# Performance work log

Hardware: AMD Instinct MI355X
Metric: run time of the kernel (lower is better)

The kernel has to match this reference:

```python
import jax, jax.numpy as jnp
import numpy as np
from jax import lax

# --- static config (matches init_kwargs) ---
K_NAT, P_NAT, NHEAD, DM, L = 5, 2, 8, 128, 3
PK, OV, STRIDE = 4, 2, 2          # patcher kernel / overlap / stride = PK-OV
PPAD = PK - OV                    # circular pad for patcher/depatcher crop
RK, RC = 5, 12                    # res layer kernel, hidden channels = 3*4
DN = ('NCHW', 'OIHW', 'NCHW')


def setup_inputs() -> dict:
    key = jax.random.key(0)
    ks = jax.random.split(key, 16)
    B, C, H, W = 2, 3, 256, 256
    rn = lambda k, shape, s=0.02: jax.random.normal(k, shape, jnp.float32) * s
    return {
        'x': jax.random.normal(ks[0], (B, C, H, W), jnp.float32),
        'pos_w': jax.random.uniform(ks[1], (C, H, W), jnp.float32) + 0.5,
        'pos_b': jax.random.uniform(ks[2], (C, H, W), jnp.float32) - 0.5,
        'patch_w': rn(ks[3], (DM, C, PK, PK), 0.05),
        'patch_b': jnp.zeros((DM,), jnp.float32),
        'ln1_g': jnp.ones((L, DM), jnp.float32),
        'ln1_b': jnp.zeros((L, DM), jnp.float32),
        'qkv_w': rn(ks[4], (L, 3 * DM, DM)),
        'qkv_b': jnp.zeros((L, 3 * DM), jnp.float32),
        'rpb': rn(ks[5], (L, NHEAD, 2 * K_NAT - 1, 2 * K_NAT - 1)),
        'proj_w': rn(ks[6], (L, DM, DM)),
        'proj_b': jnp.zeros((L, DM), jnp.float32),
        'ln2_g': jnp.ones((L, DM), jnp.float32),
        'ln2_b': jnp.zeros((L, DM), jnp.float32),
        'fc1_w': rn(ks[7], (L, 4 * DM, DM)),
        'fc1_b': jnp.zeros((L, 4 * DM), jnp.float32),
        'fc2_w': rn(ks[8], (L, DM, 4 * DM)),
        'fc2_b': jnp.zeros((L, DM), jnp.float32),
        'depatch_w': rn(ks[9], (DM, C, PK, PK), 0.05),   # ConvTranspose2d weight (Cin,Cout,kh,kw)
        'depatch_b': jnp.zeros((C,), jnp.float32),
        'res_cv1_w': rn(ks[10], (RC, C, RK, RK), 0.05),
        'res_cv1_b': jnp.zeros((RC,), jnp.float32),
        'res_cv2_w': rn(ks[11], (C, RC, 1, 1), 0.05),
        'res_cv2_b': jnp.zeros((C,), jnp.float32),
    }


def _layer_norm(x, g, b):
    m = x.mean(-1, keepdims=True)
    v = x.var(-1, keepdims=True)
    return (x - m) * lax.rsqrt(v + 1e-5) * g + b


def _nat_block(x, ln1_g, ln1_b, qkv_w, qkv_b, rpb, proj_w, proj_b,
               ln2_g, ln2_b, fc1_w, fc1_b, fc2_w, fc2_b):
    # x: (B,H,W,C). NATLayer: LN -> circular pad by k//2 -> NA -> crop -> residual -> LN -> MLP -> residual.
    # After padding, every kept (interior) pixel has a full centered kxk neighborhood,
    # so we compute q only at interior positions and gather kxk K/V windows from the padded map.
    B, H, W, C = x.shape
    k, p, h = K_NAT, P_NAT, NHEAD
    dh = C // h
    y = _layer_norm(x, ln1_g, ln1_b)
    y = jnp.pad(y, ((0, 0), (p, p), (p, p), (0, 0)), mode='wrap')  # circular
    qkv = y @ qkv_w.T + qkv_b                                      # (B,H+2p,W+2p,3C)
    q, kk, vv = jnp.split(qkv, 3, axis=-1)
    q = q[:, p:p + H, p:p + W].reshape(B, H, W, h, dh) * (dh ** -0.5)
    def win(t):
        t = t.reshape(B, H + 2 * p, W + 2 * p, h, dh)
        return jnp.stack([t[:, i:i + H, j:j + W]
                          for i in range(k) for j in range(k)], axis=3)  # (B,H,W,k*k,h,dh)
    kw, vw = win(kk), win(vv)
    bias = rpb[:, p:p + k, p:p + k].reshape(h, k * k)  # centered slice of (2k-1,2k-1) RPB
    logits = jnp.einsum('bxyhd,bxynhd->bxyhn', q, kw) + bias
    a = jax.nn.softmax(logits, axis=-1)
    o = jnp.einsum('bxyhn,bxynhd->bxyhd', a, vw).reshape(B, H, W, C)
    x = x + (o @ proj_w.T + proj_b)
    y = _layer_norm(x, ln2_g, ln2_b)
    y = jax.nn.leaky_relu(y @ fc1_w.T + fc1_b) @ fc2_w.T + fc2_b
    return x + y


def _forward(x, pos_w, pos_b, patch_w, patch_b, ln1_g, ln1_b, qkv_w, qkv_b,
             rpb, proj_w, proj_b, ln2_g, ln2_b, fc1_w, fc1_b, fc2_w, fc2_b,
             depatch_w, depatch_b, res_cv1_w, res_cv1_b, res_cv2_w, res_cv2_b):
    # positional embedding (dropout is identity, p=0)
    x = x * pos_w + pos_b
    # OverlapConvPatcher: circular pad by (PK-OV), conv kernel PK stride PK-OV -> (B,129,129,DM)
    xp = jnp.pad(x, ((0, 0), (0, 0), (PPAD, PPAD), (PPAD, PPAD)), mode='wrap')
    f = lax.conv_general_dilated(xp, patch_w, (STRIDE, STRIDE), 'VALID',
                                 dimension_numbers=DN) + patch_b[None, :, None, None]
    f = f.transpose(0, 2, 3, 1)
    for i in range(L):
        f = _nat_block(f, ln1_g[i], ln1_b[i], qkv_w[i], qkv_b[i], rpb[i],
                       proj_w[i], proj_b[i], ln2_g[i], ln2_b[i],
                       fc1_w[i], fc1_b[i], fc2_w[i], fc2_b[i])
    # OverlapDeconvDepatcher: ConvTranspose2d (kernel PK, stride PK-OV), crop PPAD border
    f = f.transpose(0, 3, 1, 2)
    wf = jnp.flip(depatch_w, (2, 3)).transpose(1, 0, 2, 3)  # (Cout,Cin,kh,kw)
    y = lax.conv_general_dilated(f, wf, (1, 1), [(PK - 1, PK - 1)] * 2,
                                 lhs_dilation=(STRIDE, STRIDE),
                                 dimension_numbers=DN) + depatch_b[None, :, None, None]
    y = y[:, :, PPAD:-PPAD, PPAD:-PPAD]  # (B,3,256,256)
    # ResLayer: circular-pad same conv 5x5 -> leaky_relu -> 1x1 conv -> residual
    yp = jnp.pad(y, ((0, 0), (0, 0), (RK // 2, RK // 2), (RK // 2, RK // 2)), mode='wrap')
    r = lax.conv_general_dilated(yp, res_cv1_w, (1, 1), 'VALID',
                                 dimension_numbers=DN) + res_cv1_b[None, :, None, None]
    r = jax.nn.leaky_relu(r)
    r = lax.conv_general_dilated(r, res_cv2_w, (1, 1), 'VALID',
                                 dimension_numbers=DN) + res_cv2_b[None, :, None, None]
    return y + r


def reference(x, pos_w, pos_b, patch_w, patch_b, ln1_g, ln1_b, qkv_w, qkv_b,
              rpb, proj_w, proj_b, ln2_g, ln2_b, fc1_w, fc1_b, fc2_w, fc2_b,
              depatch_w, depatch_b, res_cv1_w, res_cv1_b, res_cv2_w, res_cv2_b):
    return _forward(x, pos_w, pos_b, patch_w, patch_b, ln1_g, ln1_b, qkv_w, qkv_b,
                    rpb, proj_w, proj_b, ln2_g, ln2_b, fc1_w, fc1_b, fc2_w, fc2_b,
                    depatch_w, depatch_b, res_cv1_w, res_cv1_b, res_cv2_w, res_cv2_b)
```

## Files before the change

kernel.cpp:

```cpp
#include <hip/hip_runtime.h>
#include <hip/hip_bf16.h>
#include <math.h>

#define HF 129
#define WF 129
#define BDIM 2
#define TOK (BDIM*HF*WF)
#define DMOD 128
#define VTP 104

typedef __attribute__((ext_vector_type(8))) short short8;
typedef __attribute__((ext_vector_type(8))) unsigned short ushort8;
typedef __attribute__((ext_vector_type(4))) float f32x4;

__device__ __forceinline__ float leaky(float v){ return v > 0.f ? v : 0.01f*v; }
__device__ __forceinline__ float bf2f(unsigned short u){ return __uint_as_float(((unsigned int)u) << 16); }
__device__ __forceinline__ unsigned int f2bf(float f){
    unsigned int u = __float_as_uint(f);
    return (u + 0x7fff + ((u >> 16) & 1)) >> 16;
}

#define NQ 147456
#define NPJ 49152
#define N1 196608
#define N2 196608
#define NPAT 8192
#define NDEP 8192
__global__ __launch_bounds__(256) void prep_weights(
    const float* __restrict__ qkv_w, const float* __restrict__ proj_w,
    const float* __restrict__ fc1_w, const float* __restrict__ fc2_w,
    const float* __restrict__ patch_w, const float* __restrict__ dep_w,
    __hip_bfloat16* __restrict__ wq, __hip_bfloat16* __restrict__ wp,
    __hip_bfloat16* __restrict__ w1, __hip_bfloat16* __restrict__ w2,
    __hip_bfloat16* __restrict__ wpat, __hip_bfloat16* __restrict__ wdep,
    float* __restrict__ zero64)
{
    int off = blockIdx.x*256 + threadIdx.x;
    if (off < NQ) { wq[off] = __float2bfloat16(qkv_w[off]); return; } off -= NQ;
    if (off < NPJ){ wp[off] = __float2bfloat16(proj_w[off]); return; } off -= NPJ;
    if (off < N1) { w1[off] = __float2bfloat16(fc1_w[off]); return; } off -= N1;
    if (off < N2) { w2[off] = __float2bfloat16(fc2_w[off]); return; } off -= N2;
    if (off < NPAT){ int r = off>>6, e = off&63;
        wpat[off] = __float2bfloat16(e < 48 ? patch_w[r*48 + e] : 0.f); return; } off -= NPAT;
    if (off < NDEP){ int e = off>>7, d = off&127;
        wdep[off] = __float2bfloat16(e < 48 ? dep_w[d*48 + e] : 0.f); return; } off -= NDEP;
    if (off < 64) zero64[off] = 0.f;
}

__global__ __launch_bounds__(256) void im2col_kernel(
    const float* __restrict__ x, const float* __restrict__ pos_w, const float* __restrict__ pos_b,
    __hip_bfloat16* __restrict__ G)
{
    __shared__ float xs[12][260];
    int blk = blockIdx.x;
    int b = blk / HF, oh = blk - b*HF;
    int tid = threadIdx.x;
    #pragma unroll
    for (int it = 0; it < 3; ++it) {
        int p = it*4 + (tid >> 6);
        int c = p >> 2, r = p & 3;
        int h = (oh*2 + r - 2 + 256) & 255;
        int w4 = (tid & 63) * 4;
        float4 xv  = *(const float4*)(x     + ((size_t)(b*3 + c)*256 + h)*256 + w4);
        float4 pwv = *(const float4*)(pos_w + ((size_t)c*256 + h)*256 + w4);
        float4 pbv = *(const float4*)(pos_b + ((size_t)c*256 + h)*256 + w4);
        float4 o; o.x = xv.x*pwv.x + pbv.x; o.y = xv.y*pwv.y + pbv.y;
        o.z = xv.z*pwv.z + pbv.z; o.w = xv.w*pwv.w + pbv.w;
        *(float4*)&xs[p][w4] = o;
    }
    __syncthreads();
    int e = tid & 63, og = tid >> 6;
    int c = e >> 4, k = e & 15, kh = k >> 2, kw = k & 3;
    int p = c*4 + kh;
    unsigned short* Grow = (unsigned short*)G + (size_t)blk*WF*64;
    for (int ow = og; ow < WF; ow += 4) {
        unsigned short v = 0;
        if (e < 48) {
            int col = (ow*2 + kw - 2 + 256) & 255;
            v = (unsigned short)f2bf(xs[p][col]);
        }
        Grow[ow*64 + e] = v;
    }
}

template<int ACT, int RES, int OUTF, int LNE>
__global__ __launch_bounds__(256) void gemmF_kernel(
    const __hip_bfloat16* __restrict__ A, const __hip_bfloat16* __restrict__ W,
    const float* __restrict__ bias, const float* __restrict__ lng, const float* __restrict__ lnb,
    __hip_bfloat16* __restrict__ Cbf, float* __restrict__ Cf,
    __hip_bfloat16* __restrict__ yl, int M, int N, int K)
{
    __shared__ __align__(16) char As[64*128];
    __shared__ __align__(16) char Ws[128*128];
    __shared__ float2 lnred[64][2];
    int tid = threadIdx.x;
    int bm = blockIdx.x*64, bn = blockIdx.y*128;
    int lane = tid & 63, wid = tid >> 6;
    int wr = (wid >> 1)*32, wc = (wid & 1)*64;
    int lrow = lane & 15, lq = lane >> 4;
    int srow = tid >> 3, scg = tid & 7;
    int swz = (lrow & 7) << 4;
    int awo0 = ((srow     )*128 + scg*16) ^ ((srow&7)<<4);
    int awo1 = ((srow + 32)*128 + scg*16) ^ ((srow&7)<<4);

    bool v0 = (bm + srow) < M, v1 = (bm + srow + 32) < M;
    const __hip_bfloat16* a0p = A + (size_t)(bm + srow)*K + scg*8;
    const __hip_bfloat16* a1p = A + (size_t)(bm + srow + 32)*K + scg*8;
    const __hip_bfloat16* wp0 = W + (size_t)(bn + srow)*K + scg*8;

    f32x4 acc[2][4] = {};
    for (int k0 = 0; k0 < K; k0 += 64) {
        int4 va0 = {}, va1 = {};
        if (v0) va0 = *(const int4*)(a0p + k0);
        if (v1) va1 = *(const int4*)(a1p + k0);
        int4 vw0 = *(const int4*)(wp0 + k0);
        int4 vw1 = *(const int4*)(wp0 + (size_t)32*K + k0);
        int4 vw2 = *(const int4*)(wp0 + (size_t)64*K + k0);
        int4 vw3 = *(const int4*)(wp0 + (size_t)96*K + k0);
        __syncthreads();
        *(int4*)(As + awo0) = va0;
        *(int4*)(As + awo1) = va1;
        *(int4*)(Ws + awo0) = vw0;
        *(int4*)(Ws + awo1) = vw1;
        *(int4*)(Ws + (((srow+64)*128 + scg*16) ^ ((srow&7)<<4))) = vw2;
        *(int4*)(Ws + (((srow+96)*128 + scg*16) ^ ((srow&7)<<4))) = vw3;
        __syncthreads();
        #pragma unroll
        for (int ks = 0; ks < 2; ++ks) {
            int kb = ks*64;
            short8 af[2], bf[4];
            #pragma unroll
            for (int mi = 0; mi < 2; ++mi)
                af[mi] = *(const short8*)(As + (((wr + mi*16 + lrow)*128 + kb + lq*16) ^ swz));
            #pragma unroll
            for (int ni = 0; ni < 4; ++ni)
                bf[ni] = *(const short8*)(Ws + (((wc + ni*16 + lrow)*128 + kb + lq*16) ^ swz));
            #pragma unroll
            for (int mi = 0; mi < 2; ++mi)
                #pragma unroll
                for (int ni = 0; ni < 4; ++ni)
                    acc[mi][ni] = __builtin_amdgcn_mfma_f32_16x16x32_bf16(af[mi], bf[ni], acc[mi][ni], 0, 0, 0);
        }
    }
    float bcol[4];
    #pragma unroll
    for (int ni = 0; ni < 4; ++ni) bcol[ni] = bias[bn + wc + ni*16 + lrow];
    #pragma unroll
    for (int mi = 0; mi < 2; ++mi) {
        #pragma unroll
        for (int r = 0; r < 4; ++r) {
            int row = bm + wr + mi*16 + lq*4 + r;
            bool vrow = row < M;
            #pragma unroll
            for (int ni = 0; ni < 4; ++ni) {
                float v = acc[mi][ni][r] + bcol[ni];
                if (ACT) v = leaky(v);
                if (RES || OUTF) {
                    int col = wc + ni*16 + lrow;
                    size_t idx = (size_t)row*128 + col;
                    if (RES) { float old = vrow ? Cf[idx] : 0.f; v += old; }
                    if (vrow) Cf[idx] = v;
                } else {
                    int col = bn + wc + ni*16 + lrow;
                    if (vrow) Cbf[(size_t)row*N + col] = __float2bfloat16(v);
                }
                acc[mi][ni][r] = v;
            }
        }
    }
    if (LNE) {
        float sa[8], ssa[8];
        #pragma unroll
        for (int mi = 0; mi < 2; ++mi)
            #pragma unroll
            for (int r = 0; r < 4; ++r) {
                float s = 0.f, ss = 0.f;
                #pragma unroll
                for (int ni = 0; ni < 4; ++ni) { float v = acc[mi][ni][r]; s += v; ss += v*v; }
                sa[mi*4+r] = s; ssa[mi*4+r] = ss;
            }
        #pragma unroll
        for (int m = 1; m < 16; m <<= 1) {
            #pragma unroll
            for (int i = 0; i < 8; ++i) { sa[i] += __shfl_xor(sa[i], m); ssa[i] += __shfl_xor(ssa[i], m); }
        }
        if (lrow == 0) {
            #pragma unroll
            for (int i = 0; i < 8; ++i)
                lnred[wr + (i>>2)*16 + lq*4 + (i&3)][wc>>6] = make_float2(sa[i], ssa[i]);
        }
        __syncthreads();
        float gcol[4], bbcol[4];
        #pragma unroll
        for (int ni = 0; ni < 4; ++ni) {
            gcol[ni] = lng[wc + ni*16 + lrow];
            bbcol[ni] = lnb[wc + ni*16 + lrow];
        }
        #pragma unroll
        for (int mi = 0; mi < 2; ++mi) {
            #pragma unroll
            for (int r = 0; r < 4; ++r) {
                int rl = wr + mi*16 + lq*4 + r;
                int row = bm + rl;
                if (row >= M) continue;
                float2 h0 = lnred[rl][0], h1 = lnred[rl][1];
                float mean = (h0.x + h1.x) * (1.f/128.f);
                float var = (h0.y + h1.y) * (1.f/128.f) - mean*mean;
                float inv = rsqrtf(var + 1e-5f);
                #pragma unroll
                for (int ni = 0; ni < 4; ++ni) {
                    int col = wc + ni*16 + lrow;
                    float yv = (acc[mi][ni][r] - mean)*inv*gcol[ni] + bbcol[ni];
                    yl[(size_t)row*128 + col] = __float2bfloat16(yv);
                }
            }
        }
    }
}

__global__ __launch_bounds__(256) void attn_mfma_kernel(
    const __hip_bfloat16* __restrict__ qkv, const float* __restrict__ rpb,
    __hip_bfloat16* __restrict__ o)
{
    __shared__ __align__(16) char Kl[96*256];
    __shared__ __align__(16) char Vt[128*VTP*2];
    __shared__ __align__(16) char Pl[4][32*VTP*2];
    __shared__ float rpbl[8*81];
    int blk = blockIdx.x;
    int b = blk / (17*33);
    int rem = blk - b*(17*33);
    int tyi = rem / 33, txi = rem - tyi*33;
    int y0 = tyi*8, x0 = txi*4;
    int tid = threadIdx.x;
    int lane = tid & 63, wid = tid >> 6;
    int lrow = lane & 15, lq = lane >> 4;

    for (int u = tid; u < 648; u += 256) rpbl[u] = rpb[u];

    #pragma unroll
    for (int it = 0; it < 6; ++it) {
        int u = tid + it*256;
        int wtok = u >> 4, c = u & 15;
        int wy = wtok >> 3, wx = wtok & 7;
        int gy = y0 + wy - 2; gy += (gy < 0) ? HF : 0; gy -= (gy >= HF) ? HF : 0;
        int gx = x0 + wx - 2; gx += (gx < 0) ? WF : 0; gx -= (gx >= WF) ? WF : 0;
        size_t tk = (size_t)(b*HF + gy)*WF + gx;
        int4 v = *(const int4*)(qkv + tk*384 + 128 + c*8);
        *(int4*)(Kl + wtok*256 + ((c*16) ^ ((wtok & 7) << 4))) = v;
    }
    #pragma unroll
    for (int it = 0; it < 6; ++it) {
        int u = tid + it*256;
        int c = u / 96, wtok = u - c*96;
        int wy = wtok >> 3, wx = wtok & 7;
        int gy = y0 + wy - 2; gy += (gy < 0) ? HF : 0; gy -= (gy >= HF) ? HF : 0;
        int gx = x0 + wx - 2; gx += (gx < 0) ? WF : 0; gx -= (gx >= WF) ? WF : 0;
        size_t tk = (size_t)(b*HF + gy)*WF + gx;
        ushort8 v = *(const ushort8*)(qkv + tk*384 + 256 + c*8);
        unsigned short* dst = (unsigned short*)Vt + (c*8)*VTP + wtok;
        #pragma unroll
        for (int j = 0; j < 8; ++j) dst[j*VTP] = v[j];
    }
    __syncthreads();

    char* myP = Pl[wid];
    #pragma unroll
    for (int hh = 0; hh < 2; ++hh) {
        int h = wid + hh*4;
        short8 aq[2];
        #pragma unroll
        for (int mi = 0; mi < 2; ++mi) {
            int q = mi*16 + lrow;
            int ty = q >> 2, tx = q & 3;
            int gy = y0 + ty, gx = x0 + tx;
            int cy = gy < HF ? gy : HF-1, cx = gx < WF ? gx : WF-1;
            size_t tk = (size_t)(b*HF + cy)*WF + cx;
            short8 v = {};
            if (lq < 2) v = *(const short8*)(qkv + tk*384 + h*16 + lq*8);
            aq[mi] = v;
        }
        f32x4 sc[2][6];
        #pragma unroll
        for (int ni = 0; ni < 6; ++ni) {
            int krow = ni*16 + lrow;
            short8 bk = *(const short8*)(Kl + krow*256 + ((h*32 + (lq&1)*16) ^ ((krow&7)<<4)));
            f32x4 zz = {0.f,0.f,0.f,0.f};
            sc[0][ni] = __builtin_amdgcn_mfma_f32_16x16x32_bf16(aq[0], bk, zz, 0, 0, 0);
            sc[1][ni] = __builtin_amdgcn_mfma_f32_16x16x32_bf16(aq[1], bk, zz, 0, 0, 0);
        }
        int wxv = lrow & 7;
        int wyb = lrow >> 3;
        #pragma unroll
        for (int mi = 0; mi < 2; ++mi) {
            int tyq = mi*4 + lq;
            #pragma unroll
            for (int ni = 0; ni < 6; ++ni) {
                int dy = ni*2 + wyb - tyq;
                bool vdy = (dy >= 0) && (dy <= 4);
                int base = (dy + 2)*9 + wxv + 2;
                int cb = base < 3 ? 3 : (base > 80 ? 80 : base);
                const float* bp = rpbl + h*81 + cb - 3;
                float b0 = bp[0], b1 = bp[1], b2 = bp[2], b3 = bp[3];
                float bias_r[4] = {b3, b2, b1, b0};
                #pragma unroll
                for (int r = 0; r < 4; ++r) {
                    int dx = wxv - r;
                    bool ok = vdy && (dx >= 0) && (dx <= 4);
                    float s = sc[mi][ni][r]*0.25f + bias_r[r];
                    sc[mi][ni][r] = ok ? s : -1e30f;
                }
            }
        }
        float sum[8] = {};
        #pragma unroll
        for (int mi = 0; mi < 2; ++mi)
            #pragma unroll
            for (int ni = 0; ni < 6; ++ni)
                #pragma unroll
                for (int r = 0; r < 4; ++r) {
                    float p = __expf(sc[mi][ni][r]);
                    sc[mi][ni][r] = p;
                    sum[mi*4 + r] += p;
                }
        #pragma unroll
        for (int msk = 1; msk < 16; msk <<= 1)
            #pragma unroll
            for (int i = 0; i < 8; ++i) sum[i] += __shfl_xor(sum[i], msk);
        float inv[8];
        #pragma unroll
        for (int i = 0; i < 8; ++i) inv[i] = 1.f / sum[i];
        #pragma unroll
        for (int mi = 0; mi < 2; ++mi)
            #pragma unroll
            for (int ni = 0; ni < 6; ++ni)
                #pragma unroll
                for (int r = 0; r < 4; ++r) {
                    int q = mi*16 + lq*4 + r;
                    int w = ni*16 + lrow;
                    ((unsigned short*)myP)[q*VTP + w] =
                        (unsigned short)f2bf(sc[mi][ni][r]);
                }
        f32x4 ov[2] = {};
        #pragma unroll
        for (int kk = 0; kk < 3; ++kk) {
            short8 vb = *(const short8*)(Vt + (h*16 + lrow)*(VTP*2) + kk*64 + lq*16);
            #pragma unroll
            for (int mi = 0; mi < 2; ++mi) {
                short8 pa = *(const short8*)(myP + (mi*16 + lrow)*(VTP*2) + kk*64 + lq*16);
                ov[mi] = __builtin_amdgcn_mfma_f32_16x16x32_bf16(pa, vb, ov[mi], 0, 0, 0);
            }
        }
        #pragma unroll
        for (int mi = 0; mi < 2; ++mi) {
            int tyq = mi*4 + lq;
            int gy = y0 + tyq;
            #pragma unroll
            for (int r = 0; r < 4; ++r) {
                int gx = x0 + r;
                if (gy < HF && gx < WF) {
                    size_t tk = (size_t)(b*HF + gy)*WF + gx;
                    ((unsigned short*)o)[tk*128 + h*16 + lrow] =
                        (unsigned short)f2bf(ov[mi][r] * inv[mi*4 + r]);
                }
            }
        }
    }
}

template<int ACT, int RES, int OUTF, int A32>
__global__ __launch_bounds__(256) void mgemm_kernel(
    const void* __restrict__ Av, const __hip_bfloat16* __restrict__ W,
    const float* __restrict__ bias, __hip_bfloat16* __restrict__ Cbf,
    float* __restrict__ Cres, int M, int N, int K)
{
    __shared__ __align__(16) char As[64*128];
    __shared__ __align__(16) char Ws[64*128];
    int tid = threadIdx.x;
    int bm = blockIdx.x*64, bn = blockIdx.y*64;
    int lane = tid & 63, wid = tid >> 6;
    int wm = (wid >> 1)*32, wn = (wid & 1)*32;
    int lrow = lane & 15, lq = lane >> 4;
    int srow = tid >> 3, scg = tid & 7;
    int wo0 = ((srow     )*128 + scg*16) ^ ((srow&7)<<4);
    int wo1 = ((srow + 32)*128 + scg*16) ^ ((srow&7)<<4);
    int swz = (lrow & 7) << 4;
    int baseA0 = (wm + lrow     )*128 + lq*16;
    int baseA1 = (wm + 16 + lrow)*128 + lq*16;
    int baseB0 = (wn + lrow     )*128 + lq*16;
    int baseB1 = (wn + 16 + lrow)*128 + lq*16;

    f32x4 acc[2][2] = {};
    bool v0 = (bm + srow) < M, v1 = (bm + srow + 32) < M;
    const __hip_bfloat16* a0p = (const __hip_bfloat16*)Av + (size_t)(bm + srow)*K + scg*8;
    const __hip_bfloat16* a1p = (const __hip_bfloat16*)Av + (size_t)(bm + srow + 32)*K + scg*8;
    const float* a0pf = (const float*)Av + (size_t)(bm + srow)*K + scg*8;
    const float* a1pf = (const float*)Av + (size_t)(bm + srow + 32)*K + scg*8;
    const __hip_bfloat16* w0p = W + (size_t)(bn + srow)*K + scg*8;
    const __hip_bfloat16* w1p = W + (size_t)(bn + srow + 32)*K + scg*8;

    for (int k0 = 0; k0 < K; k0 += 64) {
        int4 va0 = {}, va1 = {};
        if (A32) {
            if (v0) {
                float4 p0 = *(const float4*)(a0pf + k0);
                float4 p1 = *(const float4*)(a0pf + k0 + 4);
                va0.x = (int)(f2bf(p0.x) | (f2bf(p0.y) << 16)); va0.y = (int)(f2bf(p0.z) | (f2bf(p0.w) << 16));
                va0.z = (int)(f2bf(p1.x) | (f2bf(p1.y) << 16)); va0.w = (int)(f2bf(p1.z) | (f2bf(p1.w) << 16));
            }
            if (v1) {
                float4 p0 = *(const float4*)(a1pf + k0);
                float4 p1 = *(const float4*)(a1pf + k0 + 4);
                va1.x = (int)(f2bf(p0.x) | (f2bf(p0.y) << 16)); va1.y = (int)(f2bf(p0.z) | (f2bf(p0.w) << 16));
                va1.z = (int)(f2bf(p1.x) | (f2bf(p1.y) << 16)); va1.w = (int)(f2bf(p1.z) | (f2bf(p1.w) << 16));
            }
        } else {
            if (v0) va0 = *(const int4*)(a0p + k0);
            if (v1) va1 = *(const int4*)(a1p + k0);
        }
        int4 vw0 = *(const int4*)(w0p + k0);
        int4 vw1 = *(const int4*)(w1p + k0);
        __syncthreads();
        *(int4*)(As + wo0) = va0;
        *(int4*)(As + wo1) = va1;
        *(int4*)(Ws + wo0) = vw0;
        *(int4*)(Ws + wo1) = vw1;
        __syncthreads();
        #pragma unroll
        for (int ks = 0; ks < 2; ++ks) {
            int kb = ks*64;
            short8 a0 = *(const short8*)(As + ((baseA0 + kb) ^ swz));
            short8 a1 = *(const short8*)(As + ((baseA1 + kb) ^ swz));
            short8 b0 = *(const short8*)(Ws + ((baseB0 + kb) ^ swz));
            short8 b1 = *(const short8*)(Ws + ((baseB1 + kb) ^ swz));
            acc[0][0] = __builtin_amdgcn_mfma_f32_16x16x32_bf16(a0, b0, acc[0][0], 0, 0, 0);
            acc[0][1] = __builtin_amdgcn_mfma_f32_16x16x32_bf16(a0, b1, acc[0][1], 0, 0, 0);
            acc[1][0] = __builtin_amdgcn_mfma_f32_16x16x32_bf16(a1, b0, acc[1][0], 0, 0, 0);
            acc[1][1] = __builtin_amdgcn_mfma_f32_16x16x32_bf16(a1, b1, acc[1][1], 0, 0, 0);
        }
    }
    float bv0 = bias[bn + wn + lrow];
    float bv1 = bias[bn + wn + 16 + lrow];
    #pragma unroll
    for (int mi = 0; mi < 2; ++mi) {
        #pragma unroll
        for (int r = 0; r < 4; ++r) {
            int row = bm + wm + mi*16 + lq*4 + r;
            if (row >= M) continue;
            #pragma unroll
            for (int ni = 0; ni < 2; ++ni) {
                float v = acc[mi][ni][r] + (ni ? bv1 : bv0);
                if (ACT == 1) v = leaky(v);
                int col = bn + wn + ni*16 + lrow;
                if (RES)       Cres[(size_t)row*N + col] += v;
                else if (OUTF) Cres[(size_t)row*N + col] = v;
                else           Cbf[(size_t)row*N + col] = __float2bfloat16(v);
            }
        }
    }
}

__global__ __launch_bounds__(256) void degather_kernel(const float* __restrict__ G,
    const float* __restrict__ db, float* __restrict__ yimg)
{
    int idx = blockIdx.x*256 + threadIdx.x;
    int b = idx >> 16;
    int pix = idx & 65535;
    int i = pix >> 8, j = pix & 255;
    int fh0 = i >> 1, fw0 = j >> 1;
    size_t r00 = ((size_t)(b*HF + fh0)*WF + fw0)*64;
    size_t r01 = r00 + 64;
    size_t r10 = r00 + (size_t)WF*64;
    size_t r11 = r10 + 64;
    int wr0 = (2 + (i & 1))*4, wr1 = (i & 1)*4;
    int wc0 = 2 + (j & 1), wc1 = (j & 1);
    #pragma unroll
    for (int c = 0; c < 3; ++c) {
        int e = c*16;
        float v = db[c]
                + G[r00 + e + wr0 + wc0] + G[r01 + e + wr0 + wc1]
                + G[r10 + e + wr1 + wc0] + G[r11 + e + wr1 + wc1];
        yimg[((size_t)(b*3 + c) << 16) + pix] = v;
    }
}

__global__ __launch_bounds__(256) void res_kernel(const float* __restrict__ y,
    const float* __restrict__ w1, const float* __restrict__ b1,
    const float* __restrict__ w2, const float* __restrict__ b2, float* __restrict__ out)
{
    int idx = blockIdx.x*256 + threadIdx.x;
    int b = idx >> 16;
    int pix = idx & 65535;
    int i = pix >> 8, j = pix & 255;
    float yv[3][5][5];
    #pragma unroll
    for (int c = 0; c < 3; ++c) {
        #pragma unroll
        for (int u = 0; u < 5; ++u) {
            int ii = (i + u - 2 + 256) & 255;
            #pragma unroll
            for (int v = 0; v < 5; ++v) {
                int jj = (j + v - 2 + 256) & 255;
                yv[c][u][v] = y[((size_t)(b*3 + c)*256 + ii)*256 + jj];
            }
        }
    }
    float r1[12];
    #pragma unroll
    for (int rc = 0; rc < 12; ++rc) {
        float a = b1[rc];
        #pragma unroll
        for (int c = 0; c < 3; ++c)
            #pragma unroll
            for (int u = 0; u < 5; ++u)
                #pragma unroll
                for (int v = 0; v < 5; ++v)
                    a += yv[c][u][v] * w1[rc*75 + c*25 + u*5 + v];
        r1[rc] = leaky(a);
    }
    #pragma unroll
    for (int c = 0; c < 3; ++c) {
        float a = b2[c];
        #pragma unroll
        for (int rc = 0; rc < 12; ++rc) a += r1[rc]*w2[c*12 + rc];
        out[((size_t)(b*3 + c)*256 + i)*256 + j] = yv[c][2][2] + a;
    }
}

extern "C" void kernel_launch(void* const* d_in, const int* in_sizes, int n_in,
                              void* d_out, int out_size, void* d_ws, size_t ws_size,
                              hipStream_t stream)
{
    const float* x      = (const float*)d_in[0];
    const float* pos_w  = (const float*)d_in[1];
    const float* pos_b  = (const float*)d_in[2];
    const float* patch_w= (const float*)d_in[3];
    const float* patch_b= (const float*)d_in[4];
    const float* ln1_g  = (const float*)d_in[5];
    const float* ln1_b  = (const float*)d_in[6];
    const float* qkv_w  = (const float*)d_in[7];
    const float* qkv_b  = (const float*)d_in[8];
    const float* rpb    = (const float*)d_in[9];
    const float* proj_w = (const float*)d_in[10];
    const float* proj_b = (const float*)d_in[11];
    const float* ln2_g  = (const float*)d_in[12];
    const float* ln2_b  = (const float*)d_in[13];
    const float* fc1_w  = (const float*)d_in[14];
    const float* fc1_b  = (const float*)d_in[15];
    const float* fc2_w  = (const float*)d_in[16];
    const float* fc2_b  = (const float*)d_in[17];
    const float* dep_w  = (const float*)d_in[18];
    const float* dep_b  = (const float*)d_in[19];
    const float* rc1_w  = (const float*)d_in[20];
    const float* rc1_b  = (const float*)d_in[21];
    const float* rc2_w  = (const float*)d_in[22];
    const float* rc2_b  = (const float*)d_in[23];

    const size_t SZ = (size_t)TOK * 128;
    char* w = (char*)d_ws;
    float* f            = (float*)w;            w += SZ*4;
    __hip_bfloat16* yln = (__hip_bfloat16*)w;   w += SZ*2;
    __hip_bfloat16* ao  = (__hip_bfloat16*)w;   w += SZ*2;
    __hip_bfloat16* qkvb= (__hip_bfloat16*)w;   w += (size_t)TOK*384*2;
    __hip_bfloat16* hb  = (__hip_bfloat16*)w;   w += (size_t)TOK*512*2;
    float* yimg         = (float*)w;            w += (size_t)BDIM*3*65536*4;
    __hip_bfloat16* wq  = (__hip_bfloat16*)w;   w += (size_t)NQ*2;
    __hip_bfloat16* wp  = (__hip_bfloat16*)w;   w += (size_t)NPJ*2;
    __hip_bfloat16* w1  = (__hip_bfloat16*)w;   w += (size_t)N1*2;
    __hip_bfloat16* w2  = (__hip_bfloat16*)w;   w += (size_t)N2*2;
    __hip_bfloat16* wpat= (__hip_bfloat16*)w;   w += (size_t)NPAT*2;
    __hip_bfloat16* wdep= (__hip_bfloat16*)w;   w += (size_t)NDEP*2;
    float* zero64       = (float*)w;            w += 64*4;

    __hip_bfloat16* icol = qkvb;
    float* G             = (float*)hb;

    const int PREP_TOT = NQ + NPJ + N1 + N2 + NPAT + NDEP + 64;
    prep_weights<<<(PREP_TOT + 255)/256, 256, 0, stream>>>(
        qkv_w, proj_w, fc1_w, fc2_w, patch_w, dep_w, wq, wp, w1, w2, wpat, wdep, zero64);

    im2col_kernel<<<BDIM*HF, 256, 0, stream>>>(x, pos_w, pos_b, icol);

    const int GM = (TOK + 63)/64;
    const int NTILE = 17*33*BDIM;

    gemmF_kernel<0,0,1,1><<<dim3(GM,1), 256, 0, stream>>>(icol, wpat, patch_b,
        ln1_g, ln1_b, nullptr, f, yln, TOK, 128, 64);

    for (int l = 0; l < 3; ++l) {
        gemmF_kernel<0,0,0,0><<<dim3(GM,3), 256, 0, stream>>>(yln, wq + (size_t)l*384*128,
            qkv_b + l*384, nullptr, nullptr, qkvb, nullptr, nullptr, TOK, 384, 128);
        attn_mfma_kernel<<<NTILE, 256, 0, stream>>>(qkvb, rpb + l*8*81, ao);
        gemmF_kernel<0,1,0,1><<<dim3(GM,1), 256, 0, stream>>>(ao, wp + (size_t)l*128*128,
            proj_b + l*128, ln2_g + l*128, ln2_b + l*128, nullptr, f, yln, TOK, 128, 128);
        gemmF_kernel<1,0,0,0><<<dim3(GM,4), 256, 0, stream>>>(yln, w1 + (size_t)l*512*128,
            fc1_b + l*512, nullptr, nullptr, hb, nullptr, nullptr, TOK, 512, 128);
        if (l < 2)
            gemmF_kernel<0,1,0,1><<<dim3(GM,1), 256, 0, stream>>>(hb, w2 + (size_t)l*128*512,
                fc2_b + l*128, ln1_g + (l+1)*128, ln1_b + (l+1)*128, nullptr, f, yln, TOK, 128, 512);
        else
            gemmF_kernel<0,1,0,0><<<dim3(GM,1), 256, 0, stream>>>(hb, w2 + (size_t)l*128*512,
                fc2_b + l*128, nullptr, nullptr, nullptr, f, nullptr, TOK, 128, 512);
    }

    mgemm_kernel<0,0,1,1><<<dim3(GM,1), 256, 0, stream>>>(f, wdep, zero64,
        nullptr, G, TOK, 64, 128);
    degather_kernel<<<512, 256, 0, stream>>>(G, dep_b, yimg);

    res_kernel<<<512, 256, 0, stream>>>(yimg, rc1_w, rc1_b, rc2_w, rc2_b, (float*)d_out);
}
```

Measured before the change: 331.6 us.

## Alias K/V and rpb shared buffers in attention kernel to cut LDS footprint

The neighborhood-attention kernel now computes scores and softmax for both heads first. It then reloads the same shared buffer with transposed V, and the relative-position-bias table reuses the P scratch area. This drops the kernel's static LDS use from about 80 KB to about 53 KB, so more blocks can reside per CU. In exchange it keeps both heads' score tiles live in registers, adds two extra barriers, and loads V only after the score phase instead of alongside K.

```diff
diff --git a/kernel.cpp b/kernel.cpp
--- a/kernel.cpp
+++ b/kernel.cpp
@@ -222,10 +222,9 @@
     const __hip_bfloat16* __restrict__ qkv, const float* __restrict__ rpb,
     __hip_bfloat16* __restrict__ o)
 {
-    __shared__ __align__(16) char Kl[96*256];
-    __shared__ __align__(16) char Vt[128*VTP*2];
+    __shared__ __align__(16) char KV[26624];
     __shared__ __align__(16) char Pl[4][32*VTP*2];
-    __shared__ float rpbl[8*81];
+    float* rpbl = (float*)Pl;
     int blk = blockIdx.x;
     int b = blk / (17*33);
     int rem = blk - b*(17*33);
@@ -246,24 +245,14 @@
         int gx = x0 + wx - 2; gx += (gx < 0) ? WF : 0; gx -= (gx >= WF) ? WF : 0;
         size_t tk = (size_t)(b*HF + gy)*WF + gx;
         int4 v = *(const int4*)(qkv + tk*384 + 128 + c*8);
-        *(int4*)(Kl + wtok*256 + ((c*16) ^ ((wtok & 7) << 4))) = v;
-    }
-    #pragma unroll
-    for (int it = 0; it < 6; ++it) {
-        int u = tid + it*256;
-        int c = u / 96, wtok = u - c*96;
-        int wy = wtok >> 3, wx = wtok & 7;
-        int gy = y0 + wy - 2; gy += (gy < 0) ? HF : 0; gy -= (gy >= HF) ? HF : 0;
-        int gx = x0 + wx - 2; gx += (gx < 0) ? WF : 0; gx -= (gx >= WF) ? WF : 0;
-        size_t tk = (size_t)(b*HF + gy)*WF + gx;
-        ushort8 v = *(const ushort8*)(qkv + tk*384 + 256 + c*8);
-        unsigned short* dst = (unsigned short*)Vt + (c*8)*VTP + wtok;
-        #pragma unroll
-        for (int j = 0; j < 8; ++j) dst[j*VTP] = v[j];
+        *(int4*)(KV + wtok*256 + ((c*16) ^ ((wtok & 7) << 4))) = v;
     }
     __syncthreads();
 
-    char* myP = Pl[wid];
+    f32x4 sc[2][2][6];
+    float inv[2][8];
+    int wxv = lrow & 7;
+    int wyb = lrow >> 3;
     #pragma unroll
     for (int hh = 0; hh < 2; ++hh) {
         int h = wid + hh*4;
@@ -279,17 +268,14 @@
             if (lq < 2) v = *(const short8*)(qkv + tk*384 + h*16 + lq*8);
             aq[mi] = v;
         }
-        f32x4 sc[2][6];
         #pragma unroll
         for (int ni = 0; ni < 6; ++ni) {
             int krow = ni*16 + lrow;
-            short8 bk = *(const short8*)(Kl + krow*256 + ((h*32 + (lq&1)*16) ^ ((krow&7)<<4)));
+            short8 bk = *(const short8*)(KV + krow*256 + ((h*32 + (lq&1)*16) ^ ((krow&7)<<4)));
             f32x4 zz = {0.f,0.f,0.f,0.f};
-            sc[0][ni] = __builtin_amdgcn_mfma_f32_16x16x32_bf16(aq[0], bk, zz, 0, 0, 0);
-            sc[1][ni] = __builtin_amdgcn_mfma_f32_16x16x32_bf16(aq[1], bk, zz, 0, 0, 0);
-        }
-        int wxv = lrow & 7;
-        int wyb = lrow >> 3;
+            sc[hh][0][ni] = __builtin_amdgcn_mfma_f32_16x16x32_bf16(aq[0], bk, zz, 0, 0, 0);
+            sc[hh][1][ni] = __builtin_amdgcn_mfma_f32_16x16x32_bf16(aq[1], bk, zz, 0, 0, 0);
+        }
         #pragma unroll
         for (int mi = 0; mi < 2; ++mi) {
             int tyq = mi*4 + lq;
@@ -306,8 +292,8 @@
                 for (int r = 0; r < 4; ++r) {
                     int dx = wxv - r;
                     bool ok = vdy && (dx >= 0) && (dx <= 4);
-                    float s = sc[mi][ni][r]*0.25f + bias_r[r];
-                    sc[mi][ni][r] = ok ? s : -1e30f;
+                    float s = sc[hh][mi][ni][r]*0.25f + bias_r[r];
+                    sc[hh][mi][ni][r] = ok ? s : -1e30f;
                 }
             }
         }
@@ -318,17 +304,38 @@
             for (int ni = 0; ni < 6; ++ni)
                 #pragma unroll
                 for (int r = 0; r < 4; ++r) {
-                    float p = __expf(sc[mi][ni][r]);
-                    sc[mi][ni][r] = p;
+                    float p = __expf(sc[hh][mi][ni][r]);
+                    sc[hh][mi][ni][r] = p;
                     sum[mi*4 + r] += p;
                 }
         #pragma unroll
         for (int msk = 1; msk < 16; msk <<= 1)
             #pragma unroll
             for (int i = 0; i < 8; ++i) sum[i] += __shfl_xor(sum[i], msk);
-        float inv[8];
-        #pragma unroll
-        for (int i = 0; i < 8; ++i) inv[i] = 1.f / sum[i];
+        #pragma unroll
+        for (int i = 0; i < 8; ++i) inv[hh][i] = 1.f / sum[i];
+    }
+    __syncthreads();
+
+    #pragma unroll
+    for (int it = 0; it < 6; ++it) {
+        int u = tid + it*256;
+        int c = u / 96, wtok = u - c*96;
+        int wy = wtok >> 3, wx = wtok & 7;
+        int gy = y0 + wy - 2; gy += (gy < 0) ? HF : 0; gy -= (gy >= HF) ? HF : 0;
+        int gx = x0 + wx - 2; gx += (gx < 0) ? WF : 0; gx -= (gx >= WF) ? WF : 0;
+        size_t tk = (size_t)(b*HF + gy)*WF + gx;
+        ushort8 v = *(const ushort8*)(qkv + tk*384 + 256 + c*8);
+        unsigned short* dst = (unsigned short*)KV + (c*8)*VTP + wtok;
+        #pragma unroll
+        for (int j = 0; j < 8; ++j) dst[j*VTP] = v[j];
+    }
+    __syncthreads();
+
+    char* myP = Pl[wid];
+    #pragma unroll
+    for (int hh = 0; hh < 2; ++hh) {
+        int h = wid + hh*4;
         #pragma unroll
         for (int mi = 0; mi < 2; ++mi)
             #pragma unroll
@@ -338,12 +345,12 @@
                     int q = mi*16 + lq*4 + r;
                     int w = ni*16 + lrow;
                     ((unsigned short*)myP)[q*VTP + w] =
-                        (unsigned short)f2bf(sc[mi][ni][r]);
+                        (unsigned short)f2bf(sc[hh][mi][ni][r]);
                 }
         f32x4 ov[2] = {};
         #pragma unroll
         for (int kk = 0; kk < 3; ++kk) {
-            short8 vb = *(const short8*)(Vt + (h*16 + lrow)*(VTP*2) + kk*64 + lq*16);
+            short8 vb = *(const short8*)(KV + (h*16 + lrow)*(VTP*2) + kk*64 + lq*16);
             #pragma unroll
             for (int mi = 0; mi < 2; ++mi) {
                 short8 pa = *(const short8*)(myP + (mi*16 + lrow)*(VTP*2) + kk*64 + lq*16);
@@ -360,7 +367,7 @@
                 if (gy < HF && gx < WF) {
                     size_t tk = (size_t)(b*HF + gy)*WF + gx;
                     ((unsigned short*)o)[tk*128 + h*16 + lrow] =
-                        (unsigned short)f2bf(ov[mi][r] * inv[mi*4 + r]);
+                        (unsigned short)f2bf(ov[mi][r] * inv[hh][mi*4 + r]);
                 }
             }
         }
```

Result: faster. 324.7 us (median of 2 runs) (-2.1%).
